# Kernel optimization log

Measured on AMD Instinct MI355X. Metric: run time of the kernel, lower is better.

The kernel has to match this reference:

```python
import jax, jax.numpy as jnp
import numpy as np

N_NODES = 100000
N_EDGES = 1600000
N_GRAPHS = 512
HIDDEN = 128
N_LAYERS = 3


def setup_inputs() -> dict:
    key = jax.random.key(0)
    ks = jax.random.split(key, 16)
    X = jax.random.normal(ks[0], (N_NODES, HIDDEN), dtype=jnp.float32)
    edge_index = jax.random.randint(ks[1], (2, N_EDGES), 0, N_NODES, dtype=jnp.int64)
    batch = jnp.sort(jax.random.randint(ks[2], (N_NODES,), 0, N_GRAPHS, dtype=jnp.int64))
    s = 1.0 / np.sqrt(HIDDEN)
    mlp_w1 = jax.random.normal(ks[3], (N_LAYERS, HIDDEN, HIDDEN), dtype=jnp.float32) * s
    mlp_b1 = jnp.zeros((N_LAYERS, HIDDEN), dtype=jnp.float32)
    mlp_w2 = jax.random.normal(ks[4], (N_LAYERS, HIDDEN, HIDDEN), dtype=jnp.float32) * s
    mlp_b2 = jnp.zeros((N_LAYERS, HIDDEN), dtype=jnp.float32)
    cls_w1 = jax.random.normal(ks[5], (HIDDEN * N_LAYERS, HIDDEN), dtype=jnp.float32) / np.sqrt(HIDDEN * N_LAYERS)
    cls_b1 = jnp.zeros((HIDDEN,), dtype=jnp.float32)
    cls_w2 = jax.random.normal(ks[6], (HIDDEN, HIDDEN), dtype=jnp.float32) * s
    cls_b2 = jnp.zeros((HIDDEN,), dtype=jnp.float32)
    cls_w3 = jax.random.normal(ks[7], (HIDDEN, 1), dtype=jnp.float32) * s
    cls_b3 = jnp.zeros((1,), dtype=jnp.float32)
    return {"X": X, "edge_index": edge_index, "batch": batch,
            "mlp_w1": mlp_w1, "mlp_b1": mlp_b1, "mlp_w2": mlp_w2, "mlp_b2": mlp_b2,
            "cls_w1": cls_w1, "cls_b1": cls_b1, "cls_w2": cls_w2, "cls_b2": cls_b2,
            "cls_w3": cls_w3, "cls_b3": cls_b3}


def reference(X, edge_index, batch, mlp_w1, mlp_b1, mlp_w2, mlp_b2,
              cls_w1, cls_b1, cls_w2, cls_b2, cls_w3, cls_b3):
    src, dst = edge_index[0], edge_index[1]
    xs = []
    for l in range(N_LAYERS):
        # GIN aggregation: sum_{j in N(i)} x_j ; eps = 0 so add self feature
        agg = jax.ops.segment_sum(X[src], dst, num_segments=N_NODES)  # [N, H]
        z = X + agg
        # 2-layer MLP update
        h = jax.nn.relu(z @ mlp_w1[l] + mlp_b1[l])
        h = h @ mlp_w2[l] + mlp_b2[l]
        # dropout is identity in eval; then relu
        X = jax.nn.relu(h)
        # global sum pooling per graph
        xs.append(jax.ops.segment_sum(X, batch, num_segments=N_GRAPHS))  # [G, H]
    h = jnp.concatenate(xs, axis=-1)  # JK 'cat' -> [G, H*L]
    h = jax.nn.relu(h @ cls_w1 + cls_b1)
    h = jax.nn.relu(h @ cls_w2 + cls_b2)
    logits = h @ cls_w3 + cls_b3  # [G, 1]
    return logits
```

## Files before the change

kernel.cpp:

```cpp
#include <hip/hip_runtime.h>
#include <hip/hip_fp16.h>
#include <cstddef>
#include <cstdint>

#define N_NODES   100000
#define N_EDGES   1600000
#define N_GRAPHS  512
#define HIDDEN    128
#define N_LAYERS  3

#define N_WIN        400
#define WIN_NODES    (N_NODES / N_WIN)
#define PLACE_BLOCKS 128
#define PCHUNK       (N_EDGES / PLACE_BLOCKS)

#define F2H_BLOCKS   ((N_NODES * HIDDEN / 8) / 256)
#define WCONV_BLOCKS (N_LAYERS * 2 * 16)
#define GB_BLOCKS    2
#define PREP_BLOCKS  (F2H_BLOCKS + WCONV_BLOCKS + GB_BLOCKS)

typedef _Float16 half8  __attribute__((ext_vector_type(8)));
typedef _Float16 half4v __attribute__((ext_vector_type(4)));
typedef _Float16 half2v __attribute__((ext_vector_type(2)));
typedef float    float8 __attribute__((ext_vector_type(8)));
typedef float    floatx4 __attribute__((ext_vector_type(4)));
typedef float    floatx2 __attribute__((ext_vector_type(2)));

__global__ __launch_bounds__(256) void win_count_kernel(const int* __restrict__ dst,
                                                        int* __restrict__ counts) {
    __shared__ int cs[N_WIN];
    for (int i = threadIdx.x; i < N_WIN; i += 256) cs[i] = 0;
    __syncthreads();
    const int4* d4 = (const int4*)(dst + blockIdx.x * PCHUNK);
    for (int i = threadIdx.x; i < PCHUNK / 4; i += 256) {
        int4 d = d4[i];
        atomicAdd(&cs[d.x / WIN_NODES], 1);
        atomicAdd(&cs[d.y / WIN_NODES], 1);
        atomicAdd(&cs[d.z / WIN_NODES], 1);
        atomicAdd(&cs[d.w / WIN_NODES], 1);
    }
    __syncthreads();
    for (int i = threadIdx.x; i < N_WIN; i += 256)
        counts[blockIdx.x * N_WIN + i] = cs[i];
}

__global__ __launch_bounds__(128) void win_scan1_kernel(const int* __restrict__ counts,
                                                        int* __restrict__ offsets,
                                                        int* __restrict__ colsum) {
    __shared__ int tmp[128];
    const int w = blockIdx.x;
    const int t = threadIdx.x;
    tmp[t] = counts[t * N_WIN + w];
    __syncthreads();
#pragma unroll
    for (int off = 1; off < 128; off <<= 1) {
        int u = (t >= off) ? tmp[t - off] : 0;
        __syncthreads();
        tmp[t] += u;
        __syncthreads();
    }
    offsets[t * N_WIN + w] = (t == 0) ? 0 : tmp[t - 1];
    if (t == 127) colsum[w] = tmp[127];
}

__global__ __launch_bounds__(512) void win_place_kernel(const int* __restrict__ src,
                                                        const int* __restrict__ dst,
                                                        const int* __restrict__ offsets,
                                                        const int* __restrict__ colsum,
                                                        int2* __restrict__ wedge) {
    __shared__ int ws[512];
    __shared__ int off[N_WIN];
    const int t = threadIdx.x;
    ws[t] = (t < N_WIN) ? colsum[t] : 0;
    __syncthreads();
#pragma unroll
    for (int o = 1; o < 512; o <<= 1) {
        int u = (t >= o) ? ws[t - o] : 0;
        __syncthreads();
        ws[t] += u;
        __syncthreads();
    }
    if (t < N_WIN) off[t] = offsets[blockIdx.x * N_WIN + t] + ((t == 0) ? 0 : ws[t - 1]);
    __syncthreads();
    const int4* d4 = (const int4*)(dst + blockIdx.x * PCHUNK);
    const int4* s4 = (const int4*)(src + blockIdx.x * PCHUNK);
    for (int i = t; i < PCHUNK / 4; i += 512) {
        int4 d = d4[i];
        int4 s = s4[i];
        int p0 = atomicAdd(&off[d.x / WIN_NODES], 1); wedge[p0] = make_int2(d.x, s.x);
        int p1 = atomicAdd(&off[d.y / WIN_NODES], 1); wedge[p1] = make_int2(d.y, s.y);
        int p2 = atomicAdd(&off[d.z / WIN_NODES], 1); wedge[p2] = make_int2(d.z, s.z);
        int p3 = atomicAdd(&off[d.w / WIN_NODES], 1); wedge[p3] = make_int2(d.w, s.w);
    }
}

__global__ __launch_bounds__(512) void win_csr_kernel(const int2* __restrict__ wedge,
                                                      const int* __restrict__ colsum,
                                                      int* __restrict__ row_ptr,
                                                      int* __restrict__ csr_src) {
    __shared__ int ws[512];
    __shared__ int cnt[WIN_NODES];
    __shared__ int bb[2];
    const int w = blockIdx.x, n0 = w * WIN_NODES, t = threadIdx.x;
    ws[t] = (t < N_WIN) ? colsum[t] : 0;
    __syncthreads();
#pragma unroll
    for (int o = 1; o < 512; o <<= 1) {
        int u = (t >= o) ? ws[t - o] : 0;
        __syncthreads();
        ws[t] += u;
        __syncthreads();
    }
    if (t == 0) { bb[0] = (w > 0) ? ws[w - 1] : 0; bb[1] = ws[w]; }
    if (w == N_WIN - 1 && t == 0) row_ptr[N_NODES] = ws[N_WIN - 1];
    for (int i = t; i < WIN_NODES; i += 512) cnt[i] = 0;
    __syncthreads();
    const int b0 = bb[0], b1 = bb[1];
    for (int e = b0 + t; e < b1; e += 512)
        atomicAdd(&cnt[wedge[e].x - n0], 1);
    __syncthreads();
    ws[t] = (t < WIN_NODES) ? cnt[t] : 0;
    __syncthreads();
#pragma unroll
    for (int o = 1; o < 512; o <<= 1) {
        int u = (t >= o) ? ws[t - o] : 0;
        __syncthreads();
        ws[t] += u;
        __syncthreads();
    }
    const int excl = (t == 0) ? 0 : ws[t - 1];
    if (t < WIN_NODES) {
        row_ptr[n0 + t] = b0 + excl;
        cnt[t] = b0 + excl;
    }
    __syncthreads();
    for (int e = b0 + t; e < b1; e += 512) {
        int2 ed = wedge[e];
        int p = atomicAdd(&cnt[ed.x - n0], 1);
        csr_src[p] = ed.y;
    }
}

__global__ __launch_bounds__(256) void prep_kernel(const float* __restrict__ X,
                                                   __half* __restrict__ hA,
                                                   unsigned char* __restrict__ outq,
                                                   const float* __restrict__ w1,
                                                   const float* __restrict__ w2,
                                                   __half* __restrict__ wt1,
                                                   __half* __restrict__ wt2,
                                                   const int* __restrict__ batch,
                                                   int* __restrict__ gstart) {
    __shared__ float tile[32][33];
    const int b = blockIdx.x;
    if (b < F2H_BLOCKS) {
        int t = b * 256 + threadIdx.x;
        const float4* in4 = (const float4*)X;
        float4 a = in4[t * 2 + 0];
        float4 c = in4[t * 2 + 1];
        __half2* o2 = (__half2*)hA;
        o2[t * 4 + 0] = __floats2half2_rn(a.x, a.y);
        o2[t * 4 + 1] = __floats2half2_rn(a.z, a.w);
        o2[t * 4 + 2] = __floats2half2_rn(c.x, c.y);
        o2[t * 4 + 3] = __floats2half2_rn(c.z, c.w);
        unsigned r0 = 0, r1 = 0;
        r0 = __builtin_amdgcn_cvt_pk_fp8_f32(a.x, a.y, r0, false);
        r0 = __builtin_amdgcn_cvt_pk_fp8_f32(a.z, a.w, r0, true);
        r1 = __builtin_amdgcn_cvt_pk_fp8_f32(c.x, c.y, r1, false);
        r1 = __builtin_amdgcn_cvt_pk_fp8_f32(c.z, c.w, r1, true);
        ((uint2*)outq)[t] = make_uint2(r0, r1);
    } else if (b < F2H_BLOCKS + WCONV_BLOCKS) {
        const int bb = b - F2H_BLOCKS;
        const int mat = bb & 1;
        const int tt = (bb >> 1) & 15;
        const int l  = bb >> 5;
        const int ti = (tt >> 2) * 32, tj = (tt & 3) * 32;
        const float* W = (mat ? w2 : w1) + (size_t)l * HIDDEN * HIDDEN;
        __half* WT = (mat ? wt2 : wt1) + (size_t)l * HIDDEN * HIDDEN;
        const int r = threadIdx.x >> 5;
        const int c = threadIdx.x & 31;
#pragma unroll
        for (int rr = 0; rr < 4; ++rr)
            tile[r + 8 * rr][c] = W[(size_t)(ti + r + 8 * rr) * HIDDEN + tj + c];
        __syncthreads();
#pragma unroll
        for (int rr = 0; rr < 4; ++rr)
            WT[(size_t)(tj + r + 8 * rr) * HIDDEN + ti + c] =
                __float2half(tile[c][r + 8 * rr]);
    } else {
        const int g = (b - F2H_BLOCKS - WCONV_BLOCKS) * 256 + threadIdx.x;
        if (g < N_GRAPHS) {
            int lo = 0, hi = N_NODES;
            while (lo < hi) {
                int mid = (lo + hi) >> 1;
                if (batch[mid] < g) lo = mid + 1; else hi = mid;
            }
            gstart[g] = lo;
        }
        if (g == 0) gstart[N_GRAPHS] = N_NODES;
    }
}

__device__ __forceinline__ void acc_fp8x16(float* acc, uint4 v) {
    floatx2 f;
    f = __builtin_amdgcn_cvt_pk_f32_fp8(v.x, false); acc[0] += f.x;  acc[1] += f.y;
    f = __builtin_amdgcn_cvt_pk_f32_fp8(v.x, true);  acc[2] += f.x;  acc[3] += f.y;
    f = __builtin_amdgcn_cvt_pk_f32_fp8(v.y, false); acc[4] += f.x;  acc[5] += f.y;
    f = __builtin_amdgcn_cvt_pk_f32_fp8(v.y, true);  acc[6] += f.x;  acc[7] += f.y;
    f = __builtin_amdgcn_cvt_pk_f32_fp8(v.z, false); acc[8] += f.x;  acc[9] += f.y;
    f = __builtin_amdgcn_cvt_pk_f32_fp8(v.z, true);  acc[10] += f.x; acc[11] += f.y;
    f = __builtin_amdgcn_cvt_pk_f32_fp8(v.w, false); acc[12] += f.x; acc[13] += f.y;
    f = __builtin_amdgcn_cvt_pk_f32_fp8(v.w, true);  acc[14] += f.x; acc[15] += f.y;
}

__device__ __forceinline__ void gather_body(int wave, int lane,
                                            const unsigned char* __restrict__ Xq,
                                            const __half* __restrict__ Xh,
                                            __half* __restrict__ Zh,
                                            const int* __restrict__ row_ptr,
                                            const int* __restrict__ csr_src) {
    const int grp = lane >> 3;
    const int m   = lane & 7;
    const uint4* Q = (const uint4*)Xq;

    float acc[16];
#pragma unroll
    for (int j = 0; j < 16; ++j) acc[j] = 0.f;

    int k = row_ptr[wave];
    const int end = row_ptr[wave + 1];

    for (; k + 16 <= end; k += 16) {
        int n0 = csr_src[k + grp];
        int n1 = csr_src[k + 8 + grp];
        uint4 v0 = Q[(size_t)n0 * 8 + m];
        uint4 v1 = Q[(size_t)n1 * 8 + m];
        acc_fp8x16(acc, v0);
        acc_fp8x16(acc, v1);
    }
    if (k + 8 <= end) {
        int n0 = csr_src[k + grp];
        uint4 v0 = Q[(size_t)n0 * 8 + m];
        acc_fp8x16(acc, v0);
        k += 8;
    }
    int rem = end - k;
    if (grp < rem) {
        int n0 = csr_src[k + grp];
        uint4 v0 = Q[(size_t)n0 * 8 + m];
        acc_fp8x16(acc, v0);
    }

    half2v hh[8];
#pragma unroll
    for (int j = 0; j < 8; ++j) {
        hh[j][0] = (_Float16)acc[2 * j];
        hh[j][1] = (_Float16)acc[2 * j + 1];
    }
#pragma unroll
    for (int j = 0; j < 8; ++j) {
        int b = __shfl_xor(__builtin_bit_cast(int, hh[j]), 8);
        hh[j] = hh[j] + __builtin_bit_cast(half2v, b);
    }
#pragma unroll
    for (int j = 0; j < 8; ++j) {
        int b = __shfl_xor(__builtin_bit_cast(int, hh[j]), 16);
        hh[j] = hh[j] + __builtin_bit_cast(half2v, b);
    }
#pragma unroll
    for (int j = 0; j < 8; ++j) {
        int b = __shfl_xor(__builtin_bit_cast(int, hh[j]), 32);
        hh[j] = hh[j] + __builtin_bit_cast(half2v, b);
    }

    if (grp == 0) {
        const half2v* H2 = (const half2v*)(Xh + (size_t)wave * HIDDEN + 16 * m);
        half8 o0, o1;
#pragma unroll
        for (int j = 0; j < 4; ++j) {
            half2v s = hh[j] + H2[j];
            o0[2 * j] = s[0]; o0[2 * j + 1] = s[1];
        }
#pragma unroll
        for (int j = 0; j < 4; ++j) {
            half2v s = hh[4 + j] + H2[4 + j];
            o1[2 * j] = s[0]; o1[2 * j + 1] = s[1];
        }
        ((half8*)(Zh + (size_t)wave * HIDDEN + 16 * m))[0] = o0;
        ((half8*)(Zh + (size_t)wave * HIDDEN + 16 * m))[1] = o1;
    }
}

__global__ void gather_kernel(const unsigned char* __restrict__ Xq,
                              const __half* __restrict__ Xh,
                              __half* __restrict__ Zh,
                              const int* __restrict__ row_ptr,
                              const int* __restrict__ csr_src) {
    int wave = (blockIdx.x * blockDim.x + threadIdx.x) >> 6;
    if (wave >= N_NODES) return;
    gather_body(wave, threadIdx.x & 63, Xq, Xh, Zh, row_ptr, csr_src);
}

__device__ __forceinline__ void gpool_body(int g,
                                           const __half* __restrict__ Xh,
                                           const int* __restrict__ gstart,
                                           float* __restrict__ pooled, int layer) {
    __shared__ float red[16][16][8];
    const int f8 = threadIdx.x & 15;
    const int qt = threadIdx.x >> 4;
    const int s = gstart[g], e = gstart[g + 1];

    float acc[8];
#pragma unroll
    for (int j = 0; j < 8; ++j) acc[j] = 0.f;

    for (int n = s + qt; n < e; n += 16) {
        half8 v = ((const half8*)(Xh + (size_t)n * HIDDEN))[f8];
#pragma unroll
        for (int j = 0; j < 8; ++j) acc[j] += (float)v[j];
    }
#pragma unroll
    for (int j = 0; j < 8; ++j) red[qt][f8][j] = acc[j];
    __syncthreads();

    if (threadIdx.x < 128) {
        const int c = threadIdx.x;
        float sum = 0.f;
#pragma unroll
        for (int p = 0; p < 16; ++p) sum += red[p][c >> 3][c & 7];
        pooled[(size_t)g * (HIDDEN * N_LAYERS) + layer * HIDDEN + c] = sum;
    }
}

__global__ __launch_bounds__(256) void gpool_kernel(const __half* __restrict__ Xh,
                                                    const int* __restrict__ gstart,
                                                    float* __restrict__ pooled,
                                                    int layer) {
    gpool_body(blockIdx.x, Xh, gstart, pooled, layer);
}

#define POOL_BLKS N_GRAPHS
__global__ __launch_bounds__(256) void gather_pool_kernel(const unsigned char* __restrict__ Xq,
                                                          const __half* __restrict__ Xh,
                                                          __half* __restrict__ Zh,
                                                          const int* __restrict__ row_ptr,
                                                          const int* __restrict__ csr_src,
                                                          const int* __restrict__ gstart,
                                                          float* __restrict__ pooled,
                                                          int prev_layer) {
    if (blockIdx.x < POOL_BLKS) {
        gpool_body(blockIdx.x, Xh, gstart, pooled, prev_layer);
        return;
    }
    int wave = ((blockIdx.x - POOL_BLKS) * 256 + threadIdx.x) >> 6;
    if (wave >= N_NODES) return;
    gather_body(wave, threadIdx.x & 63, Xq, Xh, Zh, row_ptr, csr_src);
}

#define MM_BLOCKS 512
__global__ __launch_bounds__(256, 2) void mlp2_kernel(const __half* __restrict__ A,
                                                      const __half* __restrict__ Wt1,
                                                      const __half* __restrict__ Wt2,
                                                      const float* __restrict__ b1,
                                                      const float* __restrict__ b2,
                                                      __half* __restrict__ C16,
                                                      unsigned char* __restrict__ Q8) {
    __shared__ __half w1s[128][128];
    __shared__ __half w2s[128][128];
    __shared__ float  bs[2][128];

    const int tid  = threadIdx.x;
    const int lane = tid & 63;
    const int m    = lane & 15;
    const int q    = lane >> 4;

    {
        const half8* s1 = (const half8*)Wt1;
        const half8* s2 = (const half8*)Wt2;
        for (int j = tid; j < 128 * 16; j += 256) {
            int r  = j >> 4;
            int cs = (j & 15) ^ (r & 15);
            *(half8*)&w1s[r][cs * 8] = s1[j];
            *(half8*)&w2s[r][cs * 8] = s2[j];
        }
        if (tid < 128) { bs[0][tid] = b1[tid]; bs[1][tid] = b2[tid]; }
    }
    __syncthreads();

    const int gwave  = (blockIdx.x * 256 + tid) >> 6;
    const int nwaves = MM_BLOCKS * 4;
    const int NTILES = N_NODES / 16;

    const int src0 = m + ((lane & 16) << 1);
    const int src1 = src0 + 16;
    const bool sel = ((lane >> 5) & 1) != 0;

    if (gwave >= NTILES) return;

    int t = gwave;
    half8 a0, a1, a2, a3;
    {
        const half8* Arow = (const half8*)(A + (size_t)(t * 16 + m) * HIDDEN);
        a0 = Arow[q]; a1 = Arow[4 + q]; a2 = Arow[8 + q]; a3 = Arow[12 + q];
    }

    while (true) {
        const int tn = t + nwaves;
        half8 n0, n1, n2, n3;
        if (tn < NTILES) {
            const half8* Nrow = (const half8*)(A + (size_t)(tn * 16 + m) * HIDDEN);
            n0 = Nrow[q]; n1 = Nrow[4 + q]; n2 = Nrow[8 + q]; n3 = Nrow[12 + q];
        }

        half8 hf[4];
#pragma unroll
        for (int c = 0; c < 4; ++c) {
            unsigned px[2], py[2];
#pragma unroll
            for (int s = 0; s < 2; ++s) {
                const int ct = 2 * c + s;
                const _Float16* wrow = (const _Float16*)&w1s[ct * 16 + m][0];
                floatx4 acc = {0.f, 0.f, 0.f, 0.f};
                acc = __builtin_amdgcn_mfma_f32_16x16x32_f16(*(const half8*)(wrow + (((0 + q) ^ m) * 8)),  a0, acc, 0, 0, 0);
                acc = __builtin_amdgcn_mfma_f32_16x16x32_f16(*(const half8*)(wrow + (((4 + q) ^ m) * 8)),  a1, acc, 0, 0, 0);
                acc = __builtin_amdgcn_mfma_f32_16x16x32_f16(*(const half8*)(wrow + (((8 + q) ^ m) * 8)),  a2, acc, 0, 0, 0);
                acc = __builtin_amdgcn_mfma_f32_16x16x32_f16(*(const half8*)(wrow + (((12 + q) ^ m) * 8)), a3, acc, 0, 0, 0);
                const floatx4 bb = *(const floatx4*)&bs[0][ct * 16 + q * 4];
                half2v p0, p1;
                p0[0] = (_Float16)fmaxf(acc[0] + bb[0], 0.f);
                p0[1] = (_Float16)fmaxf(acc[1] + bb[1], 0.f);
                p1[0] = (_Float16)fmaxf(acc[2] + bb[2], 0.f);
                p1[1] = (_Float16)fmaxf(acc[3] + bb[3], 0.f);
                px[s] = __builtin_bit_cast(unsigned, p0);
                py[s] = __builtin_bit_cast(unsigned, p1);
            }
            unsigned ax = (unsigned)__shfl((int)px[0], src0);
            unsigned ay = (unsigned)__shfl((int)py[0], src0);
            unsigned az = (unsigned)__shfl((int)px[0], src1);
            unsigned aw = (unsigned)__shfl((int)py[0], src1);
            unsigned bx = (unsigned)__shfl((int)px[1], src0);
            unsigned by = (unsigned)__shfl((int)py[1], src0);
            unsigned bz = (unsigned)__shfl((int)px[1], src1);
            unsigned bw = (unsigned)__shfl((int)py[1], src1);
            uint4 u;
            u.x = sel ? bx : ax;
            u.y = sel ? by : ay;
            u.z = sel ? bz : az;
            u.w = sel ? bw : aw;
            hf[c] = __builtin_bit_cast(half8, u);
        }

        __half* Cr = C16 + (size_t)(t * 16 + m) * HIDDEN + q * 4;
#pragma unroll
        for (int ct = 0; ct < 8; ++ct) {
            const _Float16* wrow = (const _Float16*)&w2s[ct * 16 + m][0];
            floatx4 acc = {0.f, 0.f, 0.f, 0.f};
            acc = __builtin_amdgcn_mfma_f32_16x16x32_f16(*(const half8*)(wrow + (((0 + q) ^ m) * 8)),  hf[0], acc, 0, 0, 0);
            acc = __builtin_amdgcn_mfma_f32_16x16x32_f16(*(const half8*)(wrow + (((4 + q) ^ m) * 8)),  hf[1], acc, 0, 0, 0);
            acc = __builtin_amdgcn_mfma_f32_16x16x32_f16(*(const half8*)(wrow + (((8 + q) ^ m) * 8)),  hf[2], acc, 0, 0, 0);
            acc = __builtin_amdgcn_mfma_f32_16x16x32_f16(*(const half8*)(wrow + (((12 + q) ^ m) * 8)), hf[3], acc, 0, 0, 0);
            const floatx4 bb = *(const floatx4*)&bs[1][ct * 16 + q * 4];
            float v0 = fmaxf(acc[0] + bb[0], 0.f);
            float v1 = fmaxf(acc[1] + bb[1], 0.f);
            float v2 = fmaxf(acc[2] + bb[2], 0.f);
            float v3 = fmaxf(acc[3] + bb[3], 0.f);
            half4v o;
            o[0] = (_Float16)v0; o[1] = (_Float16)v1;
            o[2] = (_Float16)v2; o[3] = (_Float16)v3;
            *(half4v*)(Cr + ct * 16) = o;
            if (Q8) {
                unsigned r0 = 0;
                r0 = __builtin_amdgcn_cvt_pk_fp8_f32(v0, v1, r0, false);
                r0 = __builtin_amdgcn_cvt_pk_fp8_f32(v2, v3, r0, true);
                *(unsigned*)(Q8 + (size_t)(t * 16 + m) * HIDDEN + ct * 16 + q * 4) = r0;
            }
        }

        if (tn >= NTILES) break;
        t = tn;
        a0 = n0; a1 = n1; a2 = n2; a3 = n3;
    }
}

__global__ __launch_bounds__(128) void cls_kernel(const float* __restrict__ pooled,
                                                  const float* __restrict__ w1,
                                                  const float* __restrict__ b1,
                                                  const float* __restrict__ w2,
                                                  const float* __restrict__ b2,
                                                  const float* __restrict__ w3,
                                                  const float* __restrict__ b3,
                                                  float* __restrict__ out) {
    __shared__ float hin[HIDDEN * N_LAYERS];
    __shared__ float h1[HIDDEN];
    __shared__ float red[HIDDEN];
    const int g = blockIdx.x;
    const int t = threadIdx.x;

    for (int i = t; i < HIDDEN * N_LAYERS; i += 128)
        hin[i] = pooled[(size_t)g * (HIDDEN * N_LAYERS) + i];
    __syncthreads();

    float s = 0.f;
    for (int k = 0; k < HIDDEN * N_LAYERS; ++k) s += hin[k] * w1[(size_t)k * HIDDEN + t];
    s = fmaxf(s + b1[t], 0.f);
    h1[t] = s;
    __syncthreads();

    float s2 = 0.f;
    for (int k = 0; k < HIDDEN; ++k) s2 += h1[k] * w2[(size_t)k * HIDDEN + t];
    s2 = fmaxf(s2 + b2[t], 0.f);

    red[t] = s2 * w3[t];
    __syncthreads();
    for (int off = 64; off > 0; off >>= 1) {
        if (t < off) red[t] += red[t + off];
        __syncthreads();
    }
    if (t == 0) out[g] = red[0] + b3[0];
}

extern "C" void kernel_launch(void* const* d_in, const int* in_sizes, int n_in,
                              void* d_out, int out_size, void* d_ws, size_t ws_size,
                              hipStream_t stream) {
    const float* X     = (const float*)d_in[0];
    const int*   ei    = (const int*)d_in[1];
    const int*   batch = (const int*)d_in[2];
    const float* w1all = (const float*)d_in[3];
    const float* b1all = (const float*)d_in[4];
    const float* w2all = (const float*)d_in[5];
    const float* b2all = (const float*)d_in[6];
    const float* cw1   = (const float*)d_in[7];
    const float* cb1   = (const float*)d_in[8];
    const float* cw2   = (const float*)d_in[9];
    const float* cb2   = (const float*)d_in[10];
    const float* cw3   = (const float*)d_in[11];
    const float* cb3   = (const float*)d_in[12];
    float* out = (float*)d_out;

    const int* src = ei;
    const int* dst = ei + N_EDGES;

    char* p = (char*)d_ws;
    auto alloc2 = [&](size_t bytes) {
        char* r = p;
        p += (bytes + 255) & ~(size_t)255;
        return r;
    };
    __half* hA      = (__half*)alloc2((size_t)N_NODES * HIDDEN * sizeof(__half));
    __half* hB      = (__half*)alloc2((size_t)N_NODES * HIDDEN * sizeof(__half));
    __half* zh      = (__half*)alloc2((size_t)N_NODES * HIDDEN * sizeof(__half));
    unsigned char* qbuf = (unsigned char*)alloc2((size_t)N_NODES * HIDDEN);
    __half* wt1     = (__half*)alloc2((size_t)N_LAYERS * HIDDEN * HIDDEN * sizeof(__half));
    __half* wt2     = (__half*)alloc2((size_t)N_LAYERS * HIDDEN * HIDDEN * sizeof(__half));
    int2*   wedge   = (int2*)alloc2((size_t)N_EDGES * sizeof(int2));
    int*    csr     = (int*)alloc2((size_t)N_EDGES * sizeof(int));
    int*    rowp    = (int*)alloc2((size_t)(N_NODES + 1) * sizeof(int));
    int*    counts  = (int*)alloc2((size_t)PLACE_BLOCKS * N_WIN * sizeof(int));
    int*    offsets = (int*)alloc2((size_t)PLACE_BLOCKS * N_WIN * sizeof(int));
    int*    colsum  = (int*)alloc2((size_t)N_WIN * sizeof(int));
    int*    gstart  = (int*)alloc2((size_t)(N_GRAPHS + 1) * sizeof(int));
    float*  pooled  = (float*)alloc2((size_t)N_GRAPHS * HIDDEN * N_LAYERS * sizeof(float));

    win_count_kernel<<<PLACE_BLOCKS, 256, 0, stream>>>(dst, counts);
    win_scan1_kernel<<<N_WIN, 128, 0, stream>>>(counts, offsets, colsum);
    win_place_kernel<<<PLACE_BLOCKS, 512, 0, stream>>>(src, dst, offsets, colsum, wedge);
    win_csr_kernel<<<N_WIN, 512, 0, stream>>>(wedge, colsum, rowp, csr);

    prep_kernel<<<PREP_BLOCKS, 256, 0, stream>>>(X, hA, qbuf, w1all, w2all, wt1, wt2,
                                                 batch, gstart);

    const int gat_grid = (N_NODES + 3) / 4;

    __half* hcur = hA;
    for (int l = 0; l < N_LAYERS; ++l) {
        __half* hnext = (l & 1) ? hA : hB;
        const bool emit = (l < N_LAYERS - 1);
        if (l == 0) {
            gather_kernel<<<gat_grid, 256, 0, stream>>>(qbuf, hcur, zh, rowp, csr);
        } else {
            gather_pool_kernel<<<gat_grid + POOL_BLKS, 256, 0, stream>>>(
                qbuf, hcur, zh, rowp, csr, gstart, pooled, l - 1);
        }
        mlp2_kernel<<<MM_BLOCKS, 256, 0, stream>>>(zh,
                                                   wt1 + (size_t)l * HIDDEN * HIDDEN,
                                                   wt2 + (size_t)l * HIDDEN * HIDDEN,
                                                   b1all + (size_t)l * HIDDEN,
                                                   b2all + (size_t)l * HIDDEN,
                                                   hnext,
                                                   emit ? qbuf : (unsigned char*)nullptr);
        hcur = hnext;
    }

    gpool_kernel<<<N_GRAPHS, 256, 0, stream>>>(hcur, gstart, pooled, N_LAYERS - 1);
    cls_kernel<<<N_GRAPHS, 128, 0, stream>>>(pooled, cw1, cb1, cw2, cb2, cw3, cb3, out);
}
```

Before: 522.7 us.

## Split fused MLP into two register-resident-weight GEMM kernels with intermediate buffer

Replaces the fused two-GEMM MLP kernel, which staged both weight matrices in LDS, with a single-GEMM kernel that is launched twice per layer. In the new kernel each wave keeps its 32-column slice of the weights and bias in registers, and all four waves of a block share one 16-row tile of A. The goal is to remove the LDS weight reads, the swizzled addressing and the cross-lane shuffles between the two GEMMs. The cost is an extra fp16 intermediate buffer of N×128 that must be written and read back through global memory, plus one more kernel launch per layer. Each wave also loads the same A tile redundantly.

Measured after the change: 462.5 us. -11.5%, faster.

```diff
diff --git a/kernel.cpp b/kernel.cpp
--- a/kernel.cpp
+++ b/kernel.cpp
@@ -356,47 +356,32 @@
     gather_body(wave, threadIdx.x & 63, Xq, Xh, Zh, row_ptr, csr_src);
 }
 
-#define MM_BLOCKS 512
-__global__ __launch_bounds__(256, 2) void mlp2_kernel(const __half* __restrict__ A,
-                                                      const __half* __restrict__ Wt1,
-                                                      const __half* __restrict__ Wt2,
-                                                      const float* __restrict__ b1,
-                                                      const float* __restrict__ b2,
-                                                      __half* __restrict__ C16,
-                                                      unsigned char* __restrict__ Q8) {
-    __shared__ __half w1s[128][128];
-    __shared__ __half w2s[128][128];
-    __shared__ float  bs[2][128];
-
+#define MM_BLOCKS 1024
+__global__ __launch_bounds__(256) void mm_ws_kernel(const __half* __restrict__ A,
+                                                    const __half* __restrict__ Wt,
+                                                    const float* __restrict__ bias,
+                                                    __half* __restrict__ C16,
+                                                    unsigned char* __restrict__ Q8) {
     const int tid  = threadIdx.x;
+    const int wid  = tid >> 6;
     const int lane = tid & 63;
     const int m    = lane & 15;
     const int q    = lane >> 4;
-
-    {
-        const half8* s1 = (const half8*)Wt1;
-        const half8* s2 = (const half8*)Wt2;
-        for (int j = tid; j < 128 * 16; j += 256) {
-            int r  = j >> 4;
-            int cs = (j & 15) ^ (r & 15);
-            *(half8*)&w1s[r][cs * 8] = s1[j];
-            *(half8*)&w2s[r][cs * 8] = s2[j];
-        }
-        if (tid < 128) { bs[0][tid] = b1[tid]; bs[1][tid] = b2[tid]; }
-    }
-    __syncthreads();
-
-    const int gwave  = (blockIdx.x * 256 + tid) >> 6;
-    const int nwaves = MM_BLOCKS * 4;
     const int NTILES = N_NODES / 16;
 
-    const int src0 = m + ((lane & 16) << 1);
-    const int src1 = src0 + 16;
-    const bool sel = ((lane >> 5) & 1) != 0;
-
-    if (gwave >= NTILES) return;
-
-    int t = gwave;
+    half8 wf[2][4];
+    float bl[2][4];
+#pragma unroll
+    for (int s = 0; s < 2; ++s) {
+        const int ct = 2 * wid + s;
+        const half8* Wrow = (const half8*)(Wt + (size_t)(ct * 16 + m) * HIDDEN);
+#pragma unroll
+        for (int c = 0; c < 4; ++c) wf[s][c] = Wrow[c * 4 + q];
+#pragma unroll
+        for (int r = 0; r < 4; ++r) bl[s][r] = bias[ct * 16 + q * 4 + r];
+    }
+
+    int t = blockIdx.x;
     half8 a0, a1, a2, a3;
     {
         const half8* Arow = (const half8*)(A + (size_t)(t * 16 + m) * HIDDEN);
@@ -404,65 +389,26 @@
     }
 
     while (true) {
-        const int tn = t + nwaves;
+        const int tn = t + MM_BLOCKS;
         half8 n0, n1, n2, n3;
         if (tn < NTILES) {
             const half8* Nrow = (const half8*)(A + (size_t)(tn * 16 + m) * HIDDEN);
             n0 = Nrow[q]; n1 = Nrow[4 + q]; n2 = Nrow[8 + q]; n3 = Nrow[12 + q];
         }
 
-        half8 hf[4];
-#pragma unroll
-        for (int c = 0; c < 4; ++c) {
-            unsigned px[2], py[2];
-#pragma unroll
-            for (int s = 0; s < 2; ++s) {
-                const int ct = 2 * c + s;
-                const _Float16* wrow = (const _Float16*)&w1s[ct * 16 + m][0];
-                floatx4 acc = {0.f, 0.f, 0.f, 0.f};
-                acc = __builtin_amdgcn_mfma_f32_16x16x32_f16(*(const half8*)(wrow + (((0 + q) ^ m) * 8)),  a0, acc, 0, 0, 0);
-                acc = __builtin_amdgcn_mfma_f32_16x16x32_f16(*(const half8*)(wrow + (((4 + q) ^ m) * 8)),  a1, acc, 0, 0, 0);
-                acc = __builtin_amdgcn_mfma_f32_16x16x32_f16(*(const half8*)(wrow + (((8 + q) ^ m) * 8)),  a2, acc, 0, 0, 0);
-                acc = __builtin_amdgcn_mfma_f32_16x16x32_f16(*(const half8*)(wrow + (((12 + q) ^ m) * 8)), a3, acc, 0, 0, 0);
-                const floatx4 bb = *(const floatx4*)&bs[0][ct * 16 + q * 4];
-                half2v p0, p1;
-                p0[0] = (_Float16)fmaxf(acc[0] + bb[0], 0.f);
-                p0[1] = (_Float16)fmaxf(acc[1] + bb[1], 0.f);
-                p1[0] = (_Float16)fmaxf(acc[2] + bb[2], 0.f);
-                p1[1] = (_Float16)fmaxf(acc[3] + bb[3], 0.f);
-                px[s] = __builtin_bit_cast(unsigned, p0);
-                py[s] = __builtin_bit_cast(unsigned, p1);
-            }
-            unsigned ax = (unsigned)__shfl((int)px[0], src0);
-            unsigned ay = (unsigned)__shfl((int)py[0], src0);
-            unsigned az = (unsigned)__shfl((int)px[0], src1);
-            unsigned aw = (unsigned)__shfl((int)py[0], src1);
-            unsigned bx = (unsigned)__shfl((int)px[1], src0);
-            unsigned by = (unsigned)__shfl((int)py[1], src0);
-            unsigned bz = (unsigned)__shfl((int)px[1], src1);
-            unsigned bw = (unsigned)__shfl((int)py[1], src1);
-            uint4 u;
-            u.x = sel ? bx : ax;
-            u.y = sel ? by : ay;
-            u.z = sel ? bz : az;
-            u.w = sel ? bw : aw;
-            hf[c] = __builtin_bit_cast(half8, u);
-        }
-
         __half* Cr = C16 + (size_t)(t * 16 + m) * HIDDEN + q * 4;
 #pragma unroll
-        for (int ct = 0; ct < 8; ++ct) {
-            const _Float16* wrow = (const _Float16*)&w2s[ct * 16 + m][0];
+        for (int s = 0; s < 2; ++s) {
+            const int ct = 2 * wid + s;
             floatx4 acc = {0.f, 0.f, 0.f, 0.f};
-            acc = __builtin_amdgcn_mfma_f32_16x16x32_f16(*(const half8*)(wrow + (((0 + q) ^ m) * 8)),  hf[0], acc, 0, 0, 0);
-            acc = __builtin_amdgcn_mfma_f32_16x16x32_f16(*(const half8*)(wrow + (((4 + q) ^ m) * 8)),  hf[1], acc, 0, 0, 0);
-            acc = __builtin_amdgcn_mfma_f32_16x16x32_f16(*(const half8*)(wrow + (((8 + q) ^ m) * 8)),  hf[2], acc, 0, 0, 0);
-            acc = __builtin_amdgcn_mfma_f32_16x16x32_f16(*(const half8*)(wrow + (((12 + q) ^ m) * 8)), hf[3], acc, 0, 0, 0);
-            const floatx4 bb = *(const floatx4*)&bs[1][ct * 16 + q * 4];
-            float v0 = fmaxf(acc[0] + bb[0], 0.f);
-            float v1 = fmaxf(acc[1] + bb[1], 0.f);
-            float v2 = fmaxf(acc[2] + bb[2], 0.f);
-            float v3 = fmaxf(acc[3] + bb[3], 0.f);
+            acc = __builtin_amdgcn_mfma_f32_16x16x32_f16(wf[s][0], a0, acc, 0, 0, 0);
+            acc = __builtin_amdgcn_mfma_f32_16x16x32_f16(wf[s][1], a1, acc, 0, 0, 0);
+            acc = __builtin_amdgcn_mfma_f32_16x16x32_f16(wf[s][2], a2, acc, 0, 0, 0);
+            acc = __builtin_amdgcn_mfma_f32_16x16x32_f16(wf[s][3], a3, acc, 0, 0, 0);
+            float v0 = fmaxf(acc[0] + bl[s][0], 0.f);
+            float v1 = fmaxf(acc[1] + bl[s][1], 0.f);
+            float v2 = fmaxf(acc[2] + bl[s][2], 0.f);
+            float v3 = fmaxf(acc[3] + bl[s][3], 0.f);
             half4v o;
             o[0] = (_Float16)v0; o[1] = (_Float16)v1;
             o[2] = (_Float16)v2; o[3] = (_Float16)v3;
@@ -548,6 +494,7 @@
     __half* hA      = (__half*)alloc2((size_t)N_NODES * HIDDEN * sizeof(__half));
     __half* hB      = (__half*)alloc2((size_t)N_NODES * HIDDEN * sizeof(__half));
     __half* zh      = (__half*)alloc2((size_t)N_NODES * HIDDEN * sizeof(__half));
+    __half* m1h     = (__half*)alloc2((size_t)N_NODES * HIDDEN * sizeof(__half));
     unsigned char* qbuf = (unsigned char*)alloc2((size_t)N_NODES * HIDDEN);
     __half* wt1     = (__half*)alloc2((size_t)N_LAYERS * HIDDEN * HIDDEN * sizeof(__half));
     __half* wt2     = (__half*)alloc2((size_t)N_LAYERS * HIDDEN * HIDDEN * sizeof(__half));
@@ -580,13 +527,15 @@
             gather_pool_kernel<<<gat_grid + POOL_BLKS, 256, 0, stream>>>(
                 qbuf, hcur, zh, rowp, csr, gstart, pooled, l - 1);
         }
-        mlp2_kernel<<<MM_BLOCKS, 256, 0, stream>>>(zh,
-                                                   wt1 + (size_t)l * HIDDEN * HIDDEN,
-                                                   wt2 + (size_t)l * HIDDEN * HIDDEN,
-                                                   b1all + (size_t)l * HIDDEN,
-                                                   b2all + (size_t)l * HIDDEN,
-                                                   hnext,
-                                                   emit ? qbuf : (unsigned char*)nullptr);
+        mm_ws_kernel<<<MM_BLOCKS, 256, 0, stream>>>(zh,
+                                                    wt1 + (size_t)l * HIDDEN * HIDDEN,
+                                                    b1all + (size_t)l * HIDDEN,
+                                                    m1h, (unsigned char*)nullptr);
+        mm_ws_kernel<<<MM_BLOCKS, 256, 0, stream>>>(m1h,
+                                                    wt2 + (size_t)l * HIDDEN * HIDDEN,
+                                                    b2all + (size_t)l * HIDDEN,
+                                                    hnext,
+                                                    emit ? qbuf : (unsigned char*)nullptr);
         hcur = hnext;
     }
 
```
